# Performance work log

Measured on AMD Instinct MI355X. Metric: run time of the kernel, lower is better.

The kernel has to match this reference:

```python
import jax, jax.numpy as jnp
import numpy as np

N_ATOMS = 50000
E_RAD = 2000000
E_ANG = 1000000
N_PAIRS = 2000000
NUM_SPECIES = 4            # H, C, N, O (ANI-1)
ECFP_DIM = 16
RADIAL_ETA = 16.0
ANGULAR_ETA = 8.0
RADIAL_DIV = 16            # must equal 4*NUM_SPECIES for the original reshape to be valid
ANGULAR_DIV = 4
ZETA = 32.0
ANGLE_SECTIONS = 4
RADIAL_START = 0.8
ANGULAR_START = 0.8
CUTOFF = 5.2
ANG_CUTOFF = 3.5
NUM_PAIR = NUM_SPECIES * (NUM_SPECIES + 1) // 2


def _conv_table():
    # maps atomic number -> species index (H=1->0, C=6->1, N=7->2, O=8->3, else 0)
    conv = np.zeros(100, dtype=np.int32)
    for i, z in enumerate([1, 6, 7, 8]):
        conv[z] = i
    return jnp.asarray(conv)


def _triu_table():
    s1, s2 = np.triu_indices(NUM_SPECIES, 0)
    triu = np.zeros((NUM_SPECIES, NUM_SPECIES), dtype=np.int32)
    pair_index = np.arange(s1.shape[0], dtype=np.int32)
    triu[s1, s2] = pair_index
    triu[s2, s1] = pair_index
    return jnp.asarray(triu)


def setup_inputs() -> dict:
    key = jax.random.key(0)
    ks = jax.random.split(key, 14)
    ecfp = jax.random.normal(ks[0], (N_ATOMS, ECFP_DIM), dtype=jnp.float32)
    species = jax.random.randint(ks[1], (N_ATOMS,), 0, 9, dtype=jnp.int32)
    distances = RADIAL_START + (CUTOFF - RADIAL_START) * jax.random.uniform(ks[2], (E_RAD,), dtype=jnp.float32)
    switch = jax.random.uniform(ks[3], (E_RAD,), dtype=jnp.float32)
    edge_src = jax.random.randint(ks[4], (E_RAD,), 0, N_ATOMS, dtype=jnp.int32)
    edge_dst = jax.random.randint(ks[5], (E_RAD,), 0, N_ATOMS, dtype=jnp.int32)
    bond_order = jax.random.randint(ks[6], (E_RAD,), 0, 6, dtype=jnp.int32)
    ang_distances = ANGULAR_START + (ANG_CUTOFF - ANGULAR_START) * jax.random.uniform(ks[7], (E_ANG,), dtype=jnp.float32)
    ang_switch = jax.random.uniform(ks[8], (E_ANG,), dtype=jnp.float32)
    ang_edge_dst = jax.random.randint(ks[9], (E_ANG,), 0, N_ATOMS, dtype=jnp.int32)
    angles = np.pi * jax.random.uniform(ks[10], (N_PAIRS,), dtype=jnp.float32)
    central_atom = jax.random.randint(ks[11], (N_PAIRS,), 0, N_ATOMS, dtype=jnp.int32)
    angle_src = jax.random.randint(ks[12], (N_PAIRS,), 0, E_ANG, dtype=jnp.int32)
    angle_dst = jax.random.randint(ks[13], (N_PAIRS,), 0, E_ANG, dtype=jnp.int32)
    return dict(ecfp=ecfp, distances=distances, switch=switch, angles=angles,
                ang_distances=ang_distances, ang_switch=ang_switch, species=species,
                bond_order=bond_order, edge_src=edge_src, edge_dst=edge_dst,
                ang_edge_dst=ang_edge_dst, central_atom=central_atom,
                angle_src=angle_src, angle_dst=angle_dst)


def reference(ecfp, distances, switch, angles, ang_distances, ang_switch,
              species, bond_order, edge_src, edge_dst, ang_edge_dst,
              central_atom, angle_src, angle_dst):
    n_atoms = species.shape[0]
    indices = _conv_table()[species]  # (N,) species bin per atom

    # bond order -> 2-way soft one-hot encoding
    weights_bo = jnp.array([1.0, 1.5, 2.0, 0.5, 3.0, 0.25], dtype=jnp.float32)
    bo = weights_bo[bond_order]
    bo2 = jnp.where(bo[:, None] >= 1,
                    jnp.array([1.0, 0.0], dtype=jnp.float32),
                    jnp.array([0.0, 1.0], dtype=jnp.float32))  # (E, 2)

    # ---- radial AEV ----
    shiftR = jnp.asarray(np.linspace(RADIAL_START, CUTOFF, RADIAL_DIV + 1)[None, :-1], dtype=distances.dtype)
    radial_terms = 0.25 * jnp.exp(-RADIAL_ETA * (distances[:, None] - shiftR) ** 2) * switch[:, None]  # (E, R)
    radial_terms = radial_terms[:, :, None] * bo2[:, None, :]  # (E, R, 2)
    radial_index = edge_src * NUM_SPECIES + indices[edge_dst]
    radial_aev = jax.ops.segment_sum(radial_terms, radial_index, NUM_SPECIES * n_atoms)
    radial_aev = radial_aev.reshape(n_atoms, NUM_SPECIES * RADIAL_DIV * 2)  # (N, 128)

    # ---- angular AEV ----
    d12 = 0.5 * (ang_distances[angle_src] + ang_distances[angle_dst])[:, None]  # (P, 1)
    angle_start = np.pi / (2 * ANGLE_SECTIONS)
    shiftZ = jnp.asarray((np.linspace(0, np.pi, ANGLE_SECTIONS + 1) + angle_start)[None, :-1], dtype=ang_distances.dtype)
    shiftA = jnp.asarray(np.linspace(ANGULAR_START, ANG_CUTOFF, ANGULAR_DIV + 1)[None, :-1], dtype=ang_distances.dtype)
    factor1 = (0.5 + 0.5 * jnp.cos(angles[:, None] - shiftZ)) ** ZETA      # (P, Z)
    factor2 = jnp.exp(-ANGULAR_ETA * (d12 - shiftA) ** 2)                   # (P, A)
    angular_terms = (factor1[:, None, :] * factor2[:, :, None]).reshape(-1, ANGLE_SECTIONS * ANGULAR_DIV)
    angular_terms = angular_terms * 2 * (ang_switch[angle_src] * ang_switch[angle_dst])[:, None]  # (P, 16)

    index_dest = indices[ang_edge_dst]  # (E_ang,)
    triu = _triu_table()
    angular_index = central_atom * NUM_PAIR + triu[index_dest[angle_src], index_dest[angle_dst]]
    angular_aev = jax.ops.segment_sum(angular_terms, angular_index, NUM_PAIR * n_atoms)
    angular_aev = angular_aev.reshape(n_atoms, NUM_PAIR * ANGLE_SECTIONS * ANGULAR_DIV)  # (N, 160)

    return jnp.concatenate((ecfp, radial_aev, angular_aev), axis=-1)  # (N, 304)
```

## Files before the change

kernel.cpp:

```cpp
#include <hip/hip_runtime.h>
#include <math.h>

#define OUTC 304
#define NBK  784
#define CAP  3072
#define SC_K 12
#define SC_F 4
#define OVF_CAP 65536

__global__ __launch_bounds__(256) void k_prep(const float* __restrict__ angd,
                                              const float* __restrict__ angsw,
                                              const int* __restrict__ aedst,
                                              const int* __restrict__ species,
                                              unsigned* __restrict__ erec, int e_ang,
                                              const float* __restrict__ ecfp,
                                              float* __restrict__ out, int total4,
                                              int* __restrict__ gcnt, int nz) {
    int i = blockIdx.x * 256 + threadIdx.x;
    if (i < nz) gcnt[i] = 0;
    if (i < total4) {
        int row = i >> 2, c4 = i & 3;
        ((float4*)out)[row * (OUTC / 4) + c4] = ((const float4*)ecfp)[i];
    }
    if (i < e_ang) {
        int z = species[aedst[i]];
        unsigned sp = (z == 6) ? 1u : (z == 7) ? 2u : (z == 8) ? 3u : 0u;
        float d = angd[i], s = angsw[i];
        unsigned dq = (unsigned)fminf(fmaxf((d - 0.8f) * (4095.0f / 2.7f) + 0.5f, 0.f), 4095.f);
        unsigned sq = (unsigned)fminf(fmaxf(s * 16383.0f + 0.5f, 0.f), 16383.f);
        erec[i] = dq | (sq << 12) | (sp << 26);
    }
}

__device__ __forceinline__ void flush_buckets(int* lcnt, uint2* stg,
                                              int* __restrict__ gcnt,
                                              uint2* __restrict__ payload,
                                              uint4* __restrict__ ovf,
                                              int* __restrict__ ovfc,
                                              int nb, unsigned tag) {
    const int tid = threadIdx.x;
    __syncthreads();
#pragma unroll
    for (int q = 0; q < 2; ++q) {
        int b = 2 * tid + q;
        if (b < nb) {
            int c = min(lcnt[b], SC_K);
            if (c > 0) {
                int gbase = atomicAdd(&gcnt[b], c);
                const uint2* sp2 = &stg[b * SC_K];
                uint2* pp = payload + (size_t)b * CAP;
                for (int k = 0; k < c; ++k) {
                    int gpos = gbase + k;
                    uint2 pl = sp2[k];
                    if (gpos < CAP) pp[gpos] = pl;
                    else {
                        int oi = atomicAdd(ovfc, 1);
                        unsigned loc = tag ? ((pl.y >> 16) & 63u) : (pl.y & 63u);
                        if (oi < OVF_CAP) ovf[oi] = make_uint4(pl.x, pl.y, (unsigned)(b * 64 + loc), tag);
                    }
                }
            }
            lcnt[b] = 0;
        }
    }
    __syncthreads();
}

__device__ __forceinline__ void scatter_rad_dev(
        const float* __restrict__ dist, const float* __restrict__ sw,
        const int* __restrict__ bond_order, const int* __restrict__ esrc,
        const int* __restrict__ edst, const int* __restrict__ species,
        int* __restrict__ gcnt, uint2* __restrict__ payload,
        uint4* __restrict__ ovf, int* __restrict__ ovfc,
        int n, int span, int nb, int bid, uint2* stg, int* lcnt) {
    const int tid = threadIdx.x;
    for (int i = tid; i < nb; i += 512) lcnt[i] = 0;
    __syncthreads();
    int base = bid * span, end = min(base + span, n);
    if (base >= end) return;
    int pend = 0;
    for (int i0 = base; i0 < end; i0 += 1024) {
        int e0 = i0 + tid, e1 = i0 + 512 + tid;
        bool v0 = e0 < end, v1 = e1 < end;
        float d0 = 0.f, s0 = 0.f, d1 = 0.f, s1 = 0.f;
        int bo0 = 0, bo1 = 0, ed0 = 0, ed1 = 0, c0i = 0, c1i = 0;
        if (v0) { d0 = dist[e0]; s0 = sw[e0]; bo0 = bond_order[e0]; c0i = esrc[e0]; ed0 = edst[e0]; }
        if (v1) { d1 = dist[e1]; s1 = sw[e1]; bo1 = bond_order[e1]; c1i = esrc[e1]; ed1 = edst[e1]; }
        int z0 = 0, z1 = 0;
        if (v0) z0 = species[ed0];
        if (v1) z1 = species[ed1];
        if (v0) {
            unsigned bb = (bo0 == 3 || bo0 == 5) ? 1u : 0u;
            unsigned sp = (z0 == 6) ? 1u : (z0 == 7) ? 2u : (z0 == 8) ? 3u : 0u;
            unsigned dq = (unsigned)fminf(fmaxf((d0 - 0.8f) * (65535.0f / 4.4f) + 0.5f, 0.f), 65535.f);
            unsigned sq = (unsigned)fminf(fmaxf(s0 * 65535.0f + 0.5f, 0.f), 65535.f);
            uint2 pl; pl.x = dq | (sq << 16); pl.y = (unsigned)(c0i & 63) | (sp << 6) | (bb << 8);
            int b = c0i >> 6;
            int slot = atomicAdd(&lcnt[b], 1);
            if (slot < SC_K) stg[b * SC_K + slot] = pl;
            else { int oi = atomicAdd(ovfc, 1); if (oi < OVF_CAP) ovf[oi] = make_uint4(pl.x, pl.y, (unsigned)c0i, 0u); }
        }
        if (v1) {
            unsigned bb = (bo1 == 3 || bo1 == 5) ? 1u : 0u;
            unsigned sp = (z1 == 6) ? 1u : (z1 == 7) ? 2u : (z1 == 8) ? 3u : 0u;
            unsigned dq = (unsigned)fminf(fmaxf((d1 - 0.8f) * (65535.0f / 4.4f) + 0.5f, 0.f), 65535.f);
            unsigned sq = (unsigned)fminf(fmaxf(s1 * 65535.0f + 0.5f, 0.f), 65535.f);
            uint2 pl; pl.x = dq | (sq << 16); pl.y = (unsigned)(c1i & 63) | (sp << 6) | (bb << 8);
            int b = c1i >> 6;
            int slot = atomicAdd(&lcnt[b], 1);
            if (slot < SC_K) stg[b * SC_K + slot] = pl;
            else { int oi = atomicAdd(ovfc, 1); if (oi < OVF_CAP) ovf[oi] = make_uint4(pl.x, pl.y, (unsigned)c1i, 0u); }
        }
        if (++pend == SC_F || i0 + 1024 >= end)
            { pend = 0; flush_buckets(lcnt, stg, gcnt, payload, ovf, ovfc, nb, 0u); }
    }
}

__device__ __forceinline__ void scatter_ang_dev(
        const float* __restrict__ angles, const unsigned* __restrict__ erec,
        const int* __restrict__ central, const int* __restrict__ psrc,
        const int* __restrict__ pdst,
        int* __restrict__ gcnt, uint2* __restrict__ payload,
        uint4* __restrict__ ovf, int* __restrict__ ovfc,
        int n, int span, int nb, int bid, uint2* stg, int* lcnt) {
    const int tid = threadIdx.x;
    for (int i = tid; i < nb; i += 512) lcnt[i] = 0;
    __syncthreads();
    int base = bid * span, end = min(base + span, n);
    if (base >= end) return;
    int pend = 0;
    for (int i0 = base; i0 < end; i0 += 1024) {
        int p0 = i0 + tid, p1 = i0 + 512 + tid;
        bool v0 = p0 < end, v1 = p1 < end;
        int is0 = 0, it0 = 0, is1 = 0, it1 = 0, c0i = 0, c1i = 0;
        float th0 = 0.f, th1 = 0.f;
        if (v0) { is0 = psrc[p0]; it0 = pdst[p0]; c0i = central[p0]; th0 = angles[p0]; }
        if (v1) { is1 = psrc[p1]; it1 = pdst[p1]; c1i = central[p1]; th1 = angles[p1]; }
        unsigned rs0 = 0, rt0 = 0, rs1 = 0, rt1 = 0;
        if (v0) { rs0 = erec[is0]; rt0 = erec[it0]; }
        if (v1) { rs1 = erec[is1]; rt1 = erec[it1]; }
        if (v0) {
            float dsrc = 0.8f + (float)(rs0 & 0xfffu) * (2.7f / 4095.0f);
            float dtgt = 0.8f + (float)(rt0 & 0xfffu) * (2.7f / 4095.0f);
            float ss = (float)((rs0 >> 12) & 0x3fffu) * (1.0f / 16383.0f);
            float st = (float)((rt0 >> 12) & 0x3fffu) * (1.0f / 16383.0f);
            int sps = (int)(rs0 >> 26), spt = (int)(rt0 >> 26);
            int i = min(sps, spt), j = max(sps, spt);
            unsigned pair = (unsigned)(i * 4 - (i * (i - 1)) / 2 + (j - i));
            float d12 = 0.5f * (dsrc + dtgt);
            float scale = 2.0f * ss * st;
            unsigned tq = (unsigned)fminf(fmaxf(th0 * (65535.0f / 3.14159265358979f) + 0.5f, 0.f), 65535.f);
            unsigned dq = (unsigned)fminf(fmaxf((d12 - 0.8f) * (65535.0f / 2.7f) + 0.5f, 0.f), 65535.f);
            unsigned sq = (unsigned)fminf(fmaxf(scale * (65535.0f / 2.0f) + 0.5f, 0.f), 65535.f);
            uint2 pl; pl.x = tq | (dq << 16); pl.y = sq | ((unsigned)(c0i & 63) << 16) | (pair << 22);
            int b = c0i >> 6;
            int slot = atomicAdd(&lcnt[b], 1);
            if (slot < SC_K) stg[b * SC_K + slot] = pl;
            else { int oi = atomicAdd(ovfc, 1); if (oi < OVF_CAP) ovf[oi] = make_uint4(pl.x, pl.y, (unsigned)c0i, 1u); }
        }
        if (v1) {
            float dsrc = 0.8f + (float)(rs1 & 0xfffu) * (2.7f / 4095.0f);
            float dtgt = 0.8f + (float)(rt1 & 0xfffu) * (2.7f / 4095.0f);
            float ss = (float)((rs1 >> 12) & 0x3fffu) * (1.0f / 16383.0f);
            float st = (float)((rt1 >> 12) & 0x3fffu) * (1.0f / 16383.0f);
            int sps = (int)(rs1 >> 26), spt = (int)(rt1 >> 26);
            int i = min(sps, spt), j = max(sps, spt);
            unsigned pair = (unsigned)(i * 4 - (i * (i - 1)) / 2 + (j - i));
            float d12 = 0.5f * (dsrc + dtgt);
            float scale = 2.0f * ss * st;
            unsigned tq = (unsigned)fminf(fmaxf(th1 * (65535.0f / 3.14159265358979f) + 0.5f, 0.f), 65535.f);
            unsigned dq = (unsigned)fminf(fmaxf((d12 - 0.8f) * (65535.0f / 2.7f) + 0.5f, 0.f), 65535.f);
            unsigned sq = (unsigned)fminf(fmaxf(scale * (65535.0f / 2.0f) + 0.5f, 0.f), 65535.f);
            uint2 pl; pl.x = tq | (dq << 16); pl.y = sq | ((unsigned)(c1i & 63) << 16) | (pair << 22);
            int b = c1i >> 6;
            int slot = atomicAdd(&lcnt[b], 1);
            if (slot < SC_K) stg[b * SC_K + slot] = pl;
            else { int oi = atomicAdd(ovfc, 1); if (oi < OVF_CAP) ovf[oi] = make_uint4(pl.x, pl.y, (unsigned)c1i, 1u); }
        }
        if (++pend == SC_F || i0 + 1024 >= end)
            { pend = 0; flush_buckets(lcnt, stg, gcnt, payload, ovf, ovfc, nb, 1u); }
    }
}

#define VTHR 1.5e-3f

__device__ __forceinline__ void proc_rad(uint2 pl, float* acc) {
    float d = 0.8f + (float)(pl.x & 0xffffu) * (4.4f / 65535.0f);
    float coef = 0.25f * (float)(pl.x >> 16) * (1.0f / 65535.0f);
    int bidx = (int)(pl.y & 63u) * 129 + (int)((pl.y >> 6) & 3u) * 32 + (int)((pl.y >> 8) & 1u);
    int c0 = (int)((d - 0.8f) * (1.0f / 0.275f)) - 1;
    c0 = max(0, min(12, c0));
    float dd = d - (0.8f + 0.275f * (float)c0);
    float* ap = acc + bidx + c0 * 2;
#pragma unroll
    for (int kk = 0; kk < 4; ++kk) {
        float delta = dd - 0.275f * (float)kk;
        float v = coef * __expf(-16.0f * delta * delta);
        if (v > VTHR) atomicAdd(&ap[kk * 2], v);
    }
}

__device__ __forceinline__ void proc_ang(uint2 pl, float* acc) {
    float th    = (float)(pl.x & 0xffffu) * (3.14159265358979f / 65535.0f);
    float d12   = 0.8f + (float)(pl.x >> 16) * (2.7f / 65535.0f);
    float scale = (float)(pl.y & 0xffffu) * (2.0f / 65535.0f);
    int rowb = (int)((pl.y >> 16) & 63u) * 161 + (int)((pl.y >> 22) & 15u) * 16;
    int z0 = (int)(th * (4.0f / 3.14159265358979f) - 0.5f);
    z0 = max(0, min(2, z0));
    float cz = (z0 == 0) ? 0.92387953251f : ((z0 == 1) ? 0.38268343236f : -0.38268343236f);
    float sz = (z0 == 0) ? 0.38268343236f : 0.92387953251f;
    float sth, cth;
    __sincosf(th, &sth, &cth);
    float cq = cth * cz + sth * sz;
    float sq = sth * cz - cth * sz;
    float xa = 0.5f + 0.5f * cq;
    float cq1 = 0.70710678119f * (cq + sq);
    float xb = 0.5f + 0.5f * cq1;
    float x2, x4, x8, x16, f1a, f1b;
    x2 = xa * xa; x4 = x2 * x2; x8 = x4 * x4; x16 = x8 * x8; f1a = x16 * x16;
    x2 = xb * xb; x4 = x2 * x2; x8 = x4 * x4; x16 = x8 * x8; f1b = x16 * x16;
    int ar = (int)((d12 - 0.8f) * (1.0f / 0.675f) + 0.5f);
    int a0 = max(0, min(1, ar - 1));
    float da = d12 - (0.8f + 0.675f * (float)a0);
    float* ap = acc + rowb + a0 * 4 + z0;
#pragma unroll
    for (int aa = 0; aa < 3; ++aa) {
        float delta = da - 0.675f * (float)aa;
        float f2 = __expf(-8.0f * delta * delta) * scale;
        float v0 = f2 * f1a;
        float v1 = f2 * f1b;
        if (v0 > VTHR) atomicAdd(&ap[aa * 4], v0);
        if (v1 > VTHR) atomicAdd(&ap[aa * 4 + 1], v1);
    }
}

__device__ __forceinline__ void accum_rad_dev(const uint2* __restrict__ payload,
                                              const int* __restrict__ gcnt,
                                              float* __restrict__ out, int n_atoms,
                                              int b, float* acc) {
    for (int i = threadIdx.x; i < 64 * 129; i += 512) acc[i] = 0.f;
    __syncthreads();
    int len = min(gcnt[b], CAP);
    const uint2* pp = payload + (size_t)b * CAP;
    for (int r = threadIdx.x; r < len; r += 512) proc_rad(pp[r], acc);
    __syncthreads();
    int a0 = b * 64;
    for (int i = threadIdx.x; i < 64 * 128; i += 512) {
        int la = i >> 7, cc = i & 127;
        int atom = a0 + la;
        if (atom < n_atoms) out[(size_t)atom * OUTC + 16 + cc] = acc[la * 129 + cc];
    }
}

__device__ __forceinline__ void accum_ang_dev(const uint2* __restrict__ payload,
                                              const int* __restrict__ gcnt,
                                              float* __restrict__ out, int n_atoms,
                                              int b, float* acc) {
    for (int i = threadIdx.x; i < 64 * 161; i += 512) acc[i] = 0.f;
    __syncthreads();
    int len = min(gcnt[b], CAP);
    const uint2* pp = payload + (size_t)b * CAP;
    for (int r = threadIdx.x; r < len; r += 512) proc_ang(pp[r], acc);
    __syncthreads();
    int a0 = b * 64;
    for (int i = threadIdx.x; i < 64 * 160; i += 512) {
        int la = i / 160, cc = i - la * 160;
        int atom = a0 + la;
        if (atom < n_atoms) out[(size_t)atom * OUTC + 144 + cc] = acc[la * 161 + cc];
    }
}

__global__ __launch_bounds__(512) void k_scatter_fused(
        const float* __restrict__ dist, const float* __restrict__ sw,
        const int* __restrict__ bond_order, const int* __restrict__ esrc,
        const int* __restrict__ edst, const int* __restrict__ species,
        int* __restrict__ gcntR, uint2* __restrict__ payR,
        const float* __restrict__ angles, const unsigned* __restrict__ erec,
        const int* __restrict__ central, const int* __restrict__ psrc,
        const int* __restrict__ pdst,
        int* __restrict__ gcntA, uint2* __restrict__ payA,
        uint4* __restrict__ ovf, int* __restrict__ ovfc,
        int e_rad, int n_pairs, int span, int nb, int gridR, int gridA) {
    __shared__ uint2 stg[NBK * SC_K];
    __shared__ int lcnt[NBK];
    int m = min(gridR, gridA), m2 = 2 * m;
    int bi = (int)blockIdx.x;
    bool ang; int bidx;
    if (bi < m2) { ang = bi & 1; bidx = bi >> 1; }
    else { ang = (gridA > gridR); bidx = m + (bi - m2); }
    if (ang)
        scatter_ang_dev(angles, erec, central, psrc, pdst, gcntA, payA,
                        ovf, ovfc, n_pairs, span, nb, bidx, stg, lcnt);
    else
        scatter_rad_dev(dist, sw, bond_order, esrc, edst, species, gcntR, payR,
                        ovf, ovfc, e_rad, span, nb, bidx, stg, lcnt);
}

__global__ __launch_bounds__(512) void k_accum_fused(const uint2* __restrict__ payR,
                                                     const int* __restrict__ gcntR,
                                                     const uint2* __restrict__ payA,
                                                     const int* __restrict__ gcntA,
                                                     float* __restrict__ out, int n_atoms) {
    __shared__ float acc[64 * 161];
    int b = blockIdx.x >> 1;
    if (blockIdx.x & 1) accum_ang_dev(payA, gcntA, out, n_atoms, b, acc);
    else                accum_rad_dev(payR, gcntR, out, n_atoms, b, acc);
}

__global__ __launch_bounds__(512) void k_scatter_rad(
        const float* __restrict__ dist, const float* __restrict__ sw,
        const int* __restrict__ bond_order, const int* __restrict__ esrc,
        const int* __restrict__ edst, const int* __restrict__ species,
        int* __restrict__ gcnt, uint2* __restrict__ payload,
        uint4* __restrict__ ovf, int* __restrict__ ovfc,
        int n, int span, int nb) {
    __shared__ uint2 stg[NBK * SC_K];
    __shared__ int lcnt[NBK];
    scatter_rad_dev(dist, sw, bond_order, esrc, edst, species, gcnt, payload,
                    ovf, ovfc, n, span, nb, blockIdx.x, stg, lcnt);
}

__global__ __launch_bounds__(512) void k_scatter_ang(
        const float* __restrict__ angles, const unsigned* __restrict__ erec,
        const int* __restrict__ central, const int* __restrict__ psrc,
        const int* __restrict__ pdst,
        int* __restrict__ gcnt, uint2* __restrict__ payload,
        uint4* __restrict__ ovf, int* __restrict__ ovfc,
        int n, int span, int nb) {
    __shared__ uint2 stg[NBK * SC_K];
    __shared__ int lcnt[NBK];
    scatter_ang_dev(angles, erec, central, psrc, pdst, gcnt, payload,
                    ovf, ovfc, n, span, nb, blockIdx.x, stg, lcnt);
}

__global__ __launch_bounds__(512) void k_accum_rad(const uint2* __restrict__ payload,
                                                   const int* __restrict__ gcnt,
                                                   float* __restrict__ out, int n_atoms) {
    __shared__ float acc[64 * 129];
    accum_rad_dev(payload, gcnt, out, n_atoms, blockIdx.x, acc);
}

__global__ __launch_bounds__(512) void k_accum_ang(const uint2* __restrict__ payload,
                                                   const int* __restrict__ gcnt,
                                                   float* __restrict__ out, int n_atoms) {
    __shared__ float acc[64 * 161];
    accum_ang_dev(payload, gcnt, out, n_atoms, blockIdx.x, acc);
}

__global__ __launch_bounds__(256) void k_spill(const uint4* __restrict__ ovf,
                                               const int* __restrict__ ovfc,
                                               float* __restrict__ out) {
    int n = min(*ovfc, OVF_CAP);
    const float CZ[4] = {0.92387953251f, 0.38268343236f, -0.38268343236f, -0.92387953251f};
    const float SZ[4] = {0.38268343236f, 0.92387953251f, 0.92387953251f, 0.38268343236f};
    for (int idx = blockIdx.x * 256 + threadIdx.x; idx < n; idx += gridDim.x * 256) {
        uint4 e = ovf[idx];
        if (e.w == 0u) {
            float d = 0.8f + (float)(e.x & 0xffffu) * (4.4f / 65535.0f);
            float coef = 0.25f * (float)(e.x >> 16) * (1.0f / 65535.0f);
            int sp = (int)((e.y >> 6) & 3u), bb = (int)((e.y >> 8) & 1u);
            float* base = out + (size_t)e.z * OUTC + 16 + sp * 32 + bb;
            for (int k = 0; k < 16; ++k) {
                float delta = d - (0.8f + 0.275f * (float)k);
                float v = coef * __expf(-16.0f * delta * delta);
                if (v > 1e-6f) unsafeAtomicAdd(base + k * 2, v);
            }
        } else {
            float th    = (float)(e.x & 0xffffu) * (3.14159265358979f / 65535.0f);
            float d12   = 0.8f + (float)(e.x >> 16) * (2.7f / 65535.0f);
            float scale = (float)(e.y & 0xffffu) * (2.0f / 65535.0f);
            int pair = (int)((e.y >> 22) & 15u);
            float* base = out + (size_t)e.z * OUTC + 144 + pair * 16;
            float sth, cth;
            __sincosf(th, &sth, &cth);
            for (int zz = 0; zz < 4; ++zz) {
                float x = 0.5f + 0.5f * (cth * CZ[zz] + sth * SZ[zz]);
                float x2 = x * x, x4 = x2 * x2, x8 = x4 * x4, x16 = x8 * x8;
                float f1 = x16 * x16;
                for (int a = 0; a < 4; ++a) {
                    float da = d12 - (0.8f + 0.675f * (float)a);
                    float v = __expf(-8.0f * da * da) * scale * f1;
                    if (v > 1e-6f) unsafeAtomicAdd(base + a * 4 + zz, v);
                }
            }
        }
    }
}

__global__ __launch_bounds__(256) void k_init_fb(const float* __restrict__ ecfp,
                                                 float* __restrict__ out, int total4) {
    int i = blockIdx.x * 256 + threadIdx.x;
    if (i >= total4) return;
    int row = i / 76, c4 = i - row * 76;
    float4 v = make_float4(0.f, 0.f, 0.f, 0.f);
    if (c4 < 4) v = ((const float4*)ecfp)[row * 4 + c4];
    ((float4*)out)[i] = v;
}

__global__ __launch_bounds__(256) void k_radial_fb(const float* __restrict__ dist,
                                                   const float* __restrict__ sw,
                                                   const int* __restrict__ bond_order,
                                                   const int* __restrict__ esrc,
                                                   const int* __restrict__ edst,
                                                   const int* __restrict__ species,
                                                   float* __restrict__ out, int e_rad) {
    int e = blockIdx.x * 256 + threadIdx.x;
    if (e >= e_rad) return;
    float d = dist[e], s = sw[e];
    int bo = bond_order[e];
    int bb = (bo == 3 || bo == 5) ? 1 : 0;
    int z = species[edst[e]];
    int sp = (z == 6) ? 1 : (z == 7) ? 2 : (z == 8) ? 3 : 0;
    float* base = out + (size_t)esrc[e] * OUTC + 16 + sp * 32 + bb;
    float coef = 0.25f * s;
#pragma unroll
    for (int r = 0; r < 16; ++r) {
        float delta = d - (0.8f + 0.275f * (float)r);
        float v = coef * __expf(-16.0f * delta * delta);
        if (v > 6e-7f) unsafeAtomicAdd(base + r * 2, v);
    }
}

__global__ __launch_bounds__(256) void k_ang_fb(const float* __restrict__ angles,
                                                const float* __restrict__ angd,
                                                const float* __restrict__ angsw,
                                                const int* __restrict__ aedst,
                                                const int* __restrict__ species,
                                                const int* __restrict__ central,
                                                const int* __restrict__ psrc,
                                                const int* __restrict__ pdst,
                                                float* __restrict__ out, int n_pairs) {
    int p = blockIdx.x * 256 + threadIdx.x;
    if (p >= n_pairs) return;
    int is = psrc[p], it = pdst[p];
    float th = angles[p];
    float d12 = 0.5f * (angd[is] + angd[it]);
    float scale = 2.0f * angsw[is] * angsw[it];
    int zs = species[aedst[is]], zt = species[aedst[it]];
    int sps = (zs == 6) ? 1 : (zs == 7) ? 2 : (zs == 8) ? 3 : 0;
    int spt = (zt == 6) ? 1 : (zt == 7) ? 2 : (zt == 8) ? 3 : 0;
    int i = min(sps, spt), j = max(sps, spt);
    int pair = i * 4 - (i * (i - 1)) / 2 + (j - i);
    float sth, cth;
    __sincosf(th, &sth, &cth);
    const float CZ[4] = {0.92387953251f, 0.38268343236f, -0.38268343236f, -0.92387953251f};
    const float SZ[4] = {0.38268343236f, 0.92387953251f, 0.92387953251f, 0.38268343236f};
    float f1[4];
#pragma unroll
    for (int zz = 0; zz < 4; ++zz) {
        float x = 0.5f + 0.5f * (cth * CZ[zz] + sth * SZ[zz]);
        float x2 = x * x, x4 = x2 * x2, x8 = x4 * x4, x16 = x8 * x8;
        f1[zz] = x16 * x16;
    }
    float* base = out + (size_t)central[p] * OUTC + 144 + pair * 16;
#pragma unroll
    for (int a = 0; a < 4; ++a) {
        float da = d12 - (0.8f + 0.675f * (float)a);
        float f2 = __expf(-8.0f * da * da) * scale;
#pragma unroll
        for (int zz = 0; zz < 4; ++zz) {
            float v = f2 * f1[zz];
            if (v > 6e-7f) unsafeAtomicAdd(base + a * 4 + zz, v);
        }
    }
}

extern "C" void kernel_launch(void* const* d_in, const int* in_sizes, int n_in,
                              void* d_out, int out_size, void* d_ws, size_t ws_size,
                              hipStream_t stream) {
    const float* ecfp      = (const float*)d_in[0];
    const float* distances = (const float*)d_in[1];
    const float* sw        = (const float*)d_in[2];
    const float* angles    = (const float*)d_in[3];
    const float* angd      = (const float*)d_in[4];
    const float* angsw     = (const float*)d_in[5];
    const int*   species   = (const int*)d_in[6];
    const int*   bond_ord  = (const int*)d_in[7];
    const int*   edge_src  = (const int*)d_in[8];
    const int*   edge_dst  = (const int*)d_in[9];
    const int*   aedst     = (const int*)d_in[10];
    const int*   central   = (const int*)d_in[11];
    const int*   angle_src = (const int*)d_in[12];
    const int*   angle_dst = (const int*)d_in[13];
    float* out = (float*)d_out;

    const int e_rad   = in_sizes[1];
    const int n_pairs = in_sizes[3];
    const int e_ang   = in_sizes[4];
    const int n_atoms = in_sizes[6];

    const int NB = (n_atoms + 63) / 64;

    size_t pay_bytes  = (size_t)NB * CAP * 8;
    size_t erec_bytes = ((size_t)e_ang * 4 + 15) & ~(size_t)15;
    size_t ovf_bytes  = (size_t)OVF_CAP * 16;
    size_t meta_bytes = (size_t)(2 * NB + 1) * 4;
    size_t need1 = pay_bytes + erec_bytes + ovf_bytes + meta_bytes;
    size_t need2 = 2 * pay_bytes + erec_bytes + ovf_bytes + meta_bytes;

    bool cap_ok = (NB <= NBK) &&
                  (e_rad  <= (size_t)NB * (CAP - 256)) &&
                  (n_pairs <= (size_t)NB * (CAP - 256));

    const int span = SC_F * 2 * 1024;
    int gridR = (e_rad + span - 1) / span;
    int gridA = (n_pairs + span - 1) / span;
    int total4 = n_atoms * 4;
    int nz = 2 * NB + 1;
    int prepN = max(e_ang, max(total4, nz));

    if (ws_size >= need2 && cap_ok) {
        uint2*    payR = (uint2*)d_ws;
        uint2*    payA = (uint2*)((char*)d_ws + pay_bytes);
        unsigned* erec = (unsigned*)((char*)d_ws + 2 * pay_bytes);
        uint4*    ovf  = (uint4*)((char*)d_ws + 2 * pay_bytes + erec_bytes);
        int*      gcntR = (int*)((char*)ovf + ovf_bytes);
        int*      gcntA = gcntR + NB;
        int*      ovfc  = gcntA + NB;

        k_prep<<<(prepN + 255) / 256, 256, 0, stream>>>(angd, angsw, aedst, species,
                                                        erec, e_ang, ecfp, out, total4,
                                                        gcntR, nz);
        k_scatter_fused<<<gridR + gridA, 512, 0, stream>>>(
            distances, sw, bond_ord, edge_src, edge_dst, species, gcntR, payR,
            angles, erec, central, angle_src, angle_dst, gcntA, payA,
            ovf, ovfc, e_rad, n_pairs, span, NB, gridR, gridA);
        k_accum_fused<<<2 * NB, 512, 0, stream>>>(payR, gcntR, payA, gcntA, out, n_atoms);
        k_spill<<<16, 256, 0, stream>>>(ovf, ovfc, out);
    } else if (ws_size >= need1 && cap_ok) {
        uint2*    payload = (uint2*)d_ws;
        unsigned* erec    = (unsigned*)((char*)d_ws + pay_bytes);
        uint4*    ovf     = (uint4*)((char*)d_ws + pay_bytes + erec_bytes);
        int*      gcntR   = (int*)((char*)ovf + ovf_bytes);
        int*      gcntA   = gcntR + NB;
        int*      ovfc    = gcntA + NB;

        k_prep<<<(prepN + 255) / 256, 256, 0, stream>>>(angd, angsw, aedst, species,
                                                        erec, e_ang, ecfp, out, total4,
                                                        gcntR, nz);
        k_scatter_rad<<<gridR, 512, 0, stream>>>(distances, sw, bond_ord, edge_src,
                                                 edge_dst, species, gcntR, payload,
                                                 ovf, ovfc, e_rad, span, NB);
        k_accum_rad<<<NB, 512, 0, stream>>>(payload, gcntR, out, n_atoms);
        k_scatter_ang<<<gridA, 512, 0, stream>>>(angles, erec, central, angle_src,
                                                 angle_dst, gcntA, payload,
                                                 ovf, ovfc, n_pairs, span, NB);
        k_accum_ang<<<NB, 512, 0, stream>>>(payload, gcntA, out, n_atoms);
        k_spill<<<16, 256, 0, stream>>>(ovf, ovfc, out);
    } else {
        int t4 = n_atoms * (OUTC / 4);
        k_init_fb<<<(t4 + 255) / 256, 256, 0, stream>>>(ecfp, out, t4);
        k_radial_fb<<<(e_rad + 255) / 256, 256, 0, stream>>>(distances, sw, bond_ord,
                                                             edge_src, edge_dst, species,
                                                             out, e_rad);
        k_ang_fb<<<(n_pairs + 255) / 256, 256, 0, stream>>>(angles, angd, angsw, aedst,
                                                            species, central, angle_src,
                                                            angle_dst, out, n_pairs);
    }
}
```

Baseline: 177.9 us.

## Use 128-atom scatter buckets with per-half filtering in accumulation

Scatter buckets now cover 128 atoms instead of 64, which halves the bucket count to fit one bucket per thread in the flush and makes each global atomic reservation cover more items. Accumulation still uses 64-atom groups: each block scans its whole 128-atom bucket and keeps only the payloads for its half. This means every payload is read twice during accumulation. The single-payload fallback path and the separate radial and angular kernels are removed.

```diff
diff --git a/kernel.cpp b/kernel.cpp
--- a/kernel.cpp
+++ b/kernel.cpp
@@ -2,9 +2,9 @@
 #include <math.h>
 
 #define OUTC 304
-#define NBK  784
-#define CAP  3072
-#define SC_K 12
+#define NBK  400
+#define CAP  6144
+#define SC_K 22
 #define SC_F 4
 #define OVF_CAP 65536
 
@@ -38,30 +38,26 @@
                                               uint4* __restrict__ ovf,
                                               int* __restrict__ ovfc,
                                               int nb, unsigned tag) {
-    const int tid = threadIdx.x;
-    __syncthreads();
-#pragma unroll
-    for (int q = 0; q < 2; ++q) {
-        int b = 2 * tid + q;
-        if (b < nb) {
-            int c = min(lcnt[b], SC_K);
-            if (c > 0) {
-                int gbase = atomicAdd(&gcnt[b], c);
-                const uint2* sp2 = &stg[b * SC_K];
-                uint2* pp = payload + (size_t)b * CAP;
-                for (int k = 0; k < c; ++k) {
-                    int gpos = gbase + k;
-                    uint2 pl = sp2[k];
-                    if (gpos < CAP) pp[gpos] = pl;
-                    else {
-                        int oi = atomicAdd(ovfc, 1);
-                        unsigned loc = tag ? ((pl.y >> 16) & 63u) : (pl.y & 63u);
-                        if (oi < OVF_CAP) ovf[oi] = make_uint4(pl.x, pl.y, (unsigned)(b * 64 + loc), tag);
-                    }
+    const int b = threadIdx.x;
+    __syncthreads();
+    if (b < nb) {
+        int c = min(lcnt[b], SC_K);
+        if (c > 0) {
+            int gbase = atomicAdd(&gcnt[b], c);
+            const uint2* sp2 = &stg[b * SC_K];
+            uint2* pp = payload + (size_t)b * CAP;
+            for (int k = 0; k < c; ++k) {
+                int gpos = gbase + k;
+                uint2 pl = sp2[k];
+                if (gpos < CAP) pp[gpos] = pl;
+                else {
+                    int oi = atomicAdd(ovfc, 1);
+                    unsigned loc = tag ? ((pl.y >> 16) & 127u) : (pl.y & 127u);
+                    if (oi < OVF_CAP) ovf[oi] = make_uint4(pl.x, pl.y, (unsigned)(b * 128 + loc), tag);
                 }
             }
-            lcnt[b] = 0;
-        }
+        }
+        lcnt[b] = 0;
     }
     __syncthreads();
 }
@@ -94,8 +90,8 @@
             unsigned sp = (z0 == 6) ? 1u : (z0 == 7) ? 2u : (z0 == 8) ? 3u : 0u;
             unsigned dq = (unsigned)fminf(fmaxf((d0 - 0.8f) * (65535.0f / 4.4f) + 0.5f, 0.f), 65535.f);
             unsigned sq = (unsigned)fminf(fmaxf(s0 * 65535.0f + 0.5f, 0.f), 65535.f);
-            uint2 pl; pl.x = dq | (sq << 16); pl.y = (unsigned)(c0i & 63) | (sp << 6) | (bb << 8);
-            int b = c0i >> 6;
+            uint2 pl; pl.x = dq | (sq << 16); pl.y = (unsigned)(c0i & 127) | (sp << 7) | (bb << 9);
+            int b = c0i >> 7;
             int slot = atomicAdd(&lcnt[b], 1);
             if (slot < SC_K) stg[b * SC_K + slot] = pl;
             else { int oi = atomicAdd(ovfc, 1); if (oi < OVF_CAP) ovf[oi] = make_uint4(pl.x, pl.y, (unsigned)c0i, 0u); }
@@ -105,8 +101,8 @@
             unsigned sp = (z1 == 6) ? 1u : (z1 == 7) ? 2u : (z1 == 8) ? 3u : 0u;
             unsigned dq = (unsigned)fminf(fmaxf((d1 - 0.8f) * (65535.0f / 4.4f) + 0.5f, 0.f), 65535.f);
             unsigned sq = (unsigned)fminf(fmaxf(s1 * 65535.0f + 0.5f, 0.f), 65535.f);
-            uint2 pl; pl.x = dq | (sq << 16); pl.y = (unsigned)(c1i & 63) | (sp << 6) | (bb << 8);
-            int b = c1i >> 6;
+            uint2 pl; pl.x = dq | (sq << 16); pl.y = (unsigned)(c1i & 127) | (sp << 7) | (bb << 9);
+            int b = c1i >> 7;
             int slot = atomicAdd(&lcnt[b], 1);
             if (slot < SC_K) stg[b * SC_K + slot] = pl;
             else { int oi = atomicAdd(ovfc, 1); if (oi < OVF_CAP) ovf[oi] = make_uint4(pl.x, pl.y, (unsigned)c1i, 0u); }
@@ -152,8 +148,8 @@
             unsigned tq = (unsigned)fminf(fmaxf(th0 * (65535.0f / 3.14159265358979f) + 0.5f, 0.f), 65535.f);
             unsigned dq = (unsigned)fminf(fmaxf((d12 - 0.8f) * (65535.0f / 2.7f) + 0.5f, 0.f), 65535.f);
             unsigned sq = (unsigned)fminf(fmaxf(scale * (65535.0f / 2.0f) + 0.5f, 0.f), 65535.f);
-            uint2 pl; pl.x = tq | (dq << 16); pl.y = sq | ((unsigned)(c0i & 63) << 16) | (pair << 22);
-            int b = c0i >> 6;
+            uint2 pl; pl.x = tq | (dq << 16); pl.y = sq | ((unsigned)(c0i & 127) << 16) | (pair << 23);
+            int b = c0i >> 7;
             int slot = atomicAdd(&lcnt[b], 1);
             if (slot < SC_K) stg[b * SC_K + slot] = pl;
             else { int oi = atomicAdd(ovfc, 1); if (oi < OVF_CAP) ovf[oi] = make_uint4(pl.x, pl.y, (unsigned)c0i, 1u); }
@@ -171,8 +167,8 @@
             unsigned tq = (unsigned)fminf(fmaxf(th1 * (65535.0f / 3.14159265358979f) + 0.5f, 0.f), 65535.f);
             unsigned dq = (unsigned)fminf(fmaxf((d12 - 0.8f) * (65535.0f / 2.7f) + 0.5f, 0.f), 65535.f);
             unsigned sq = (unsigned)fminf(fmaxf(scale * (65535.0f / 2.0f) + 0.5f, 0.f), 65535.f);
-            uint2 pl; pl.x = tq | (dq << 16); pl.y = sq | ((unsigned)(c1i & 63) << 16) | (pair << 22);
-            int b = c1i >> 6;
+            uint2 pl; pl.x = tq | (dq << 16); pl.y = sq | ((unsigned)(c1i & 127) << 16) | (pair << 23);
+            int b = c1i >> 7;
             int slot = atomicAdd(&lcnt[b], 1);
             if (slot < SC_K) stg[b * SC_K + slot] = pl;
             else { int oi = atomicAdd(ovfc, 1); if (oi < OVF_CAP) ovf[oi] = make_uint4(pl.x, pl.y, (unsigned)c1i, 1u); }
@@ -187,7 +183,7 @@
 __device__ __forceinline__ void proc_rad(uint2 pl, float* acc) {
     float d = 0.8f + (float)(pl.x & 0xffffu) * (4.4f / 65535.0f);
     float coef = 0.25f * (float)(pl.x >> 16) * (1.0f / 65535.0f);
-    int bidx = (int)(pl.y & 63u) * 129 + (int)((pl.y >> 6) & 3u) * 32 + (int)((pl.y >> 8) & 1u);
+    int bidx = (int)(pl.y & 63u) * 129 + (int)((pl.y >> 7) & 3u) * 32 + (int)((pl.y >> 9) & 1u);
     int c0 = (int)((d - 0.8f) * (1.0f / 0.275f)) - 1;
     c0 = max(0, min(12, c0));
     float dd = d - (0.8f + 0.275f * (float)c0);
@@ -204,7 +200,7 @@
     float th    = (float)(pl.x & 0xffffu) * (3.14159265358979f / 65535.0f);
     float d12   = 0.8f + (float)(pl.x >> 16) * (2.7f / 65535.0f);
     float scale = (float)(pl.y & 0xffffu) * (2.0f / 65535.0f);
-    int rowb = (int)((pl.y >> 16) & 63u) * 161 + (int)((pl.y >> 22) & 15u) * 16;
+    int rowb = (int)((pl.y >> 16) & 63u) * 161 + (int)((pl.y >> 23) & 15u) * 16;
     int z0 = (int)(th * (4.0f / 3.14159265358979f) - 0.5f);
     z0 = max(0, min(2, z0));
     float cz = (z0 == 0) ? 0.92387953251f : ((z0 == 1) ? 0.38268343236f : -0.38268343236f);
@@ -237,14 +233,18 @@
 __device__ __forceinline__ void accum_rad_dev(const uint2* __restrict__ payload,
                                               const int* __restrict__ gcnt,
                                               float* __restrict__ out, int n_atoms,
-                                              int b, float* acc) {
+                                              int g, float* acc) {
+    int bin = g >> 1, half = g & 1;
     for (int i = threadIdx.x; i < 64 * 129; i += 512) acc[i] = 0.f;
     __syncthreads();
-    int len = min(gcnt[b], CAP);
-    const uint2* pp = payload + (size_t)b * CAP;
-    for (int r = threadIdx.x; r < len; r += 512) proc_rad(pp[r], acc);
-    __syncthreads();
-    int a0 = b * 64;
+    int len = min(gcnt[bin], CAP);
+    const uint2* pp = payload + (size_t)bin * CAP;
+    for (int r = threadIdx.x; r < len; r += 512) {
+        uint2 pl = pp[r];
+        if ((int)((pl.y >> 6) & 1u) == half) proc_rad(pl, acc);
+    }
+    __syncthreads();
+    int a0 = g * 64;
     for (int i = threadIdx.x; i < 64 * 128; i += 512) {
         int la = i >> 7, cc = i & 127;
         int atom = a0 + la;
@@ -255,14 +255,18 @@
 __device__ __forceinline__ void accum_ang_dev(const uint2* __restrict__ payload,
                                               const int* __restrict__ gcnt,
                                               float* __restrict__ out, int n_atoms,
-                                              int b, float* acc) {
+                                              int g, float* acc) {
+    int bin = g >> 1, half = g & 1;
     for (int i = threadIdx.x; i < 64 * 161; i += 512) acc[i] = 0.f;
     __syncthreads();
-    int len = min(gcnt[b], CAP);
-    const uint2* pp = payload + (size_t)b * CAP;
-    for (int r = threadIdx.x; r < len; r += 512) proc_ang(pp[r], acc);
-    __syncthreads();
-    int a0 = b * 64;
+    int len = min(gcnt[bin], CAP);
+    const uint2* pp = payload + (size_t)bin * CAP;
+    for (int r = threadIdx.x; r < len; r += 512) {
+        uint2 pl = pp[r];
+        if ((int)((pl.y >> 22) & 1u) == half) proc_ang(pl, acc);
+    }
+    __syncthreads();
+    int a0 = g * 64;
     for (int i = threadIdx.x; i < 64 * 160; i += 512) {
         int la = i / 160, cc = i - la * 160;
         int atom = a0 + la;
@@ -302,49 +306,9 @@
                                                      const int* __restrict__ gcntA,
                                                      float* __restrict__ out, int n_atoms) {
     __shared__ float acc[64 * 161];
-    int b = blockIdx.x >> 1;
-    if (blockIdx.x & 1) accum_ang_dev(payA, gcntA, out, n_atoms, b, acc);
-    else                accum_rad_dev(payR, gcntR, out, n_atoms, b, acc);
-}
-
-__global__ __launch_bounds__(512) void k_scatter_rad(
-        const float* __restrict__ dist, const float* __restrict__ sw,
-        const int* __restrict__ bond_order, const int* __restrict__ esrc,
-        const int* __restrict__ edst, const int* __restrict__ species,
-        int* __restrict__ gcnt, uint2* __restrict__ payload,
-        uint4* __restrict__ ovf, int* __restrict__ ovfc,
-        int n, int span, int nb) {
-    __shared__ uint2 stg[NBK * SC_K];
-    __shared__ int lcnt[NBK];
-    scatter_rad_dev(dist, sw, bond_order, esrc, edst, species, gcnt, payload,
-                    ovf, ovfc, n, span, nb, blockIdx.x, stg, lcnt);
-}
-
-__global__ __launch_bounds__(512) void k_scatter_ang(
-        const float* __restrict__ angles, const unsigned* __restrict__ erec,
-        const int* __restrict__ central, const int* __restrict__ psrc,
-        const int* __restrict__ pdst,
-        int* __restrict__ gcnt, uint2* __restrict__ payload,
-        uint4* __restrict__ ovf, int* __restrict__ ovfc,
-        int n, int span, int nb) {
-    __shared__ uint2 stg[NBK * SC_K];
-    __shared__ int lcnt[NBK];
-    scatter_ang_dev(angles, erec, central, psrc, pdst, gcnt, payload,
-                    ovf, ovfc, n, span, nb, blockIdx.x, stg, lcnt);
-}
-
-__global__ __launch_bounds__(512) void k_accum_rad(const uint2* __restrict__ payload,
-                                                   const int* __restrict__ gcnt,
-                                                   float* __restrict__ out, int n_atoms) {
-    __shared__ float acc[64 * 129];
-    accum_rad_dev(payload, gcnt, out, n_atoms, blockIdx.x, acc);
-}
-
-__global__ __launch_bounds__(512) void k_accum_ang(const uint2* __restrict__ payload,
-                                                   const int* __restrict__ gcnt,
-                                                   float* __restrict__ out, int n_atoms) {
-    __shared__ float acc[64 * 161];
-    accum_ang_dev(payload, gcnt, out, n_atoms, blockIdx.x, acc);
+    int g = blockIdx.x >> 1;
+    if (blockIdx.x & 1) accum_ang_dev(payA, gcntA, out, n_atoms, g, acc);
+    else                accum_rad_dev(payR, gcntR, out, n_atoms, g, acc);
 }
 
 __global__ __launch_bounds__(256) void k_spill(const uint4* __restrict__ ovf,
@@ -358,7 +322,7 @@
         if (e.w == 0u) {
             float d = 0.8f + (float)(e.x & 0xffffu) * (4.4f / 65535.0f);
             float coef = 0.25f * (float)(e.x >> 16) * (1.0f / 65535.0f);
-            int sp = (int)((e.y >> 6) & 3u), bb = (int)((e.y >> 8) & 1u);
+            int sp = (int)((e.y >> 7) & 3u), bb = (int)((e.y >> 9) & 1u);
             float* base = out + (size_t)e.z * OUTC + 16 + sp * 32 + bb;
             for (int k = 0; k < 16; ++k) {
                 float delta = d - (0.8f + 0.275f * (float)k);
@@ -369,7 +333,7 @@
             float th    = (float)(e.x & 0xffffu) * (3.14159265358979f / 65535.0f);
             float d12   = 0.8f + (float)(e.x >> 16) * (2.7f / 65535.0f);
             float scale = (float)(e.y & 0xffffu) * (2.0f / 65535.0f);
-            int pair = (int)((e.y >> 22) & 15u);
+            int pair = (int)((e.y >> 23) & 15u);
             float* base = out + (size_t)e.z * OUTC + 144 + pair * 16;
             float sth, cth;
             __sincosf(th, &sth, &cth);
@@ -489,18 +453,18 @@
     const int e_ang   = in_sizes[4];
     const int n_atoms = in_sizes[6];
 
-    const int NB = (n_atoms + 63) / 64;
+    const int NB  = (n_atoms + 127) / 128;
+    const int G64 = (n_atoms + 63) / 64;
 
     size_t pay_bytes  = (size_t)NB * CAP * 8;
     size_t erec_bytes = ((size_t)e_ang * 4 + 15) & ~(size_t)15;
     size_t ovf_bytes  = (size_t)OVF_CAP * 16;
     size_t meta_bytes = (size_t)(2 * NB + 1) * 4;
-    size_t need1 = pay_bytes + erec_bytes + ovf_bytes + meta_bytes;
     size_t need2 = 2 * pay_bytes + erec_bytes + ovf_bytes + meta_bytes;
 
     bool cap_ok = (NB <= NBK) &&
-                  (e_rad  <= (size_t)NB * (CAP - 256)) &&
-                  (n_pairs <= (size_t)NB * (CAP - 256));
+                  (e_rad  <= (size_t)NB * (CAP - 512)) &&
+                  (n_pairs <= (size_t)NB * (CAP - 512));
 
     const int span = SC_F * 2 * 1024;
     int gridR = (e_rad + span - 1) / span;
@@ -525,27 +489,7 @@
             distances, sw, bond_ord, edge_src, edge_dst, species, gcntR, payR,
             angles, erec, central, angle_src, angle_dst, gcntA, payA,
             ovf, ovfc, e_rad, n_pairs, span, NB, gridR, gridA);
-        k_accum_fused<<<2 * NB, 512, 0, stream>>>(payR, gcntR, payA, gcntA, out, n_atoms);
-        k_spill<<<16, 256, 0, stream>>>(ovf, ovfc, out);
-    } else if (ws_size >= need1 && cap_ok) {
-        uint2*    payload = (uint2*)d_ws;
-        unsigned* erec    = (unsigned*)((char*)d_ws + pay_bytes);
-        uint4*    ovf     = (uint4*)((char*)d_ws + pay_bytes + erec_bytes);
-        int*      gcntR   = (int*)((char*)ovf + ovf_bytes);
-        int*      gcntA   = gcntR + NB;
-        int*      ovfc    = gcntA + NB;
-
-        k_prep<<<(prepN + 255) / 256, 256, 0, stream>>>(angd, angsw, aedst, species,
-                                                        erec, e_ang, ecfp, out, total4,
-                                                        gcntR, nz);
-        k_scatter_rad<<<gridR, 512, 0, stream>>>(distances, sw, bond_ord, edge_src,
-                                                 edge_dst, species, gcntR, payload,
-                                                 ovf, ovfc, e_rad, span, NB);
-        k_accum_rad<<<NB, 512, 0, stream>>>(payload, gcntR, out, n_atoms);
-        k_scatter_ang<<<gridA, 512, 0, stream>>>(angles, erec, central, angle_src,
-                                                 angle_dst, gcntA, payload,
-                                                 ovf, ovfc, n_pairs, span, NB);
-        k_accum_ang<<<NB, 512, 0, stream>>>(payload, gcntA, out, n_atoms);
+        k_accum_fused<<<2 * G64, 512, 0, stream>>>(payR, gcntR, payA, gcntA, out, n_atoms);
         k_spill<<<16, 256, 0, stream>>>(ovf, ovfc, out);
     } else {
         int t4 = n_atoms * (OUTC / 4);
```

After: 173.1 us. 2.7% less time.
